# Optimization experiments

Hardware: AMD Instinct MI355X
Metric: run time of the kernel (lower is better)

## Reference

```python
import jax, jax.numpy as jnp
import numpy as np

KS, ST, PD = 4, 2, 1
AZI = 2.0 * np.pi / 1024.0
INC = 0.0073
C_IN, C_OUT = 64, 128


def _buffers():
    # torch: cos_azi[sh, sw] = cos(azi * (sw - ks//2)); cos_inc[sh, sw] = cos(inc * (sh - ks//2))
    d = np.arange(KS, dtype=np.float32) - KS // 2
    cos_azi = np.broadcast_to(np.cos(AZI * d)[None, :], (KS, KS))
    sin_azi = np.broadcast_to(np.sin(AZI * d)[None, :], (KS, KS))
    cos_inc = np.broadcast_to(np.cos(INC * d)[:, None], (KS, KS))
    sin_inc = np.broadcast_to(np.sin(INC * d)[:, None], (KS, KS))
    shp = (1, 1, 1, 1, KS, KS)
    return tuple(jnp.asarray(np.ascontiguousarray(b).reshape(shp), jnp.float32)
                 for b in (cos_azi, sin_azi, cos_inc, sin_inc))


def _pad(a, w_value):
    # pad width with constant, then height circularly (matches F.pad order in torch code)
    a = jnp.pad(a, ((0, 0), (0, 0), (0, 0), (PD, PD)), constant_values=w_value)
    return jnp.pad(a, ((0, 0), (0, 0), (PD, PD), (0, 0)), mode='wrap')


def _unfold(a):
    # torch a.unfold(3, ks, st).unfold(2, ks, st) -> [B,C,Ho,Wo,kw,kh]
    B, C, Hp, Wp = a.shape
    Ho = (Hp - KS) // ST + 1
    Wo = (Wp - KS) // ST + 1
    ih = (ST * jnp.arange(Ho))[:, None] + jnp.arange(KS)  # [Ho, ks]
    iw = (ST * jnp.arange(Wo))[:, None] + jnp.arange(KS)  # [Wo, ks]
    p = a[:, :, ih[:, None, :, None], iw[None, :, None, :]]  # [B,C,Ho,Wo,kh,kw]
    return jnp.transpose(p, (0, 1, 2, 3, 5, 4))               # [B,C,Ho,Wo,kw,kh]


def _forward(x, r, W1, b1, W2, b2, Wc, bc):
    cos_azi, sin_azi, cos_inc, sin_inc = _buffers()
    rp = _unfold(_pad(r, 100.0))                      # [B,1,Ho,Wo,kw,kh]
    r_center = rp[:, :, :, :, KS // 2, KS // 2]       # [B,1,Ho,Wo]
    pe0 = rp * cos_azi * cos_inc - r_center[..., None, None]
    pe1 = rp * cos_azi * sin_inc
    pe2 = rp * sin_azi
    pe = jnp.concatenate([pe0, pe1, pe2], axis=1)     # [B,3,Ho,Wo,kw,kh]
    pe = jnp.transpose(pe, (0, 2, 3, 4, 5, 1))        # [B,Ho,Wo,kw,kh,3]
    h = jax.nn.leaky_relu(pe @ W1 + b1, 0.2)          # [B,Ho,Wo,kw,kh,C]
    w = h @ W2 + b2                                   # [B,Ho,Wo,kw,kh,C]
    w = jnp.transpose(w, (0, 5, 1, 2, 3, 4))          # [B,C,Ho,Wo,kw,kh]
    xp = _unfold(_pad(x, 0.0)) * w                    # [B,C,Ho,Wo,kw,kh]
    B, C, Ho, Wo = xp.shape[:4]
    xp = jnp.transpose(xp, (0, 1, 4, 5, 2, 3)).reshape(B, C * KS * KS, Ho, Wo)
    out = jnp.einsum('bkhw,ok->bohw', xp, Wc) + bc[None, :, None, None]
    return out, r_center


def setup_inputs() -> dict:
    key = jax.random.key(0)
    ks = jax.random.split(key, 8)
    B, H, W = 4, 64, 1024
    x = jax.random.normal(ks[0], (B, C_IN, H, W), jnp.float32)
    r = jax.random.uniform(ks[1], (B, 1, H, W), jnp.float32) * 50.0  # metres
    W1 = jax.random.normal(ks[2], (3, C_IN), jnp.float32) * 0.3
    b1 = jax.random.normal(ks[3], (C_IN,), jnp.float32) * 0.02
    W2 = jax.random.normal(ks[4], (C_IN, C_IN), jnp.float32) * (1.0 / np.sqrt(C_IN))
    b2 = jax.random.normal(ks[5], (C_IN,), jnp.float32) * 0.02
    Wc = jax.random.normal(ks[6], (C_OUT, C_IN * KS * KS), jnp.float32) * (1.0 / np.sqrt(C_IN * KS * KS))
    bc = jax.random.normal(ks[7], (C_OUT,), jnp.float32) * 0.02
    return {'x': x, 'r': r, 'W1': W1, 'b1': b1, 'W2': W2, 'b2': b2, 'Wc': Wc, 'bc': bc}


def reference(x, r, W1, b1, W2, b2, Wc, bc):
    return _forward(x, r, W1, b1, W2, b2, Wc, bc)
```

## Files before the change

### kernel.cpp

```cpp
#include <hip/hip_runtime.h>
#include <hip/hip_bf16.h>

namespace {

constexpr int B_   = 4;
constexpr int CIN  = 64;
constexpr int COUT = 128;
constexpr int HIN  = 64,  WIN  = 1024;
constexpr int HOUT = 32,  WOUT = 512;
constexpr int TW   = 16;
constexpr int SP   = 1096;
constexpr int KTOT = CIN * 16;

typedef __bf16 bf16x8 __attribute__((ext_vector_type(8)));
typedef float  f32x4  __attribute__((ext_vector_type(4)));

__global__ void cvt_wts(const float* __restrict__ Wc, const float* __restrict__ W2,
                        __hip_bfloat16* __restrict__ wcb, __hip_bfloat16* __restrict__ w2t) {
    int i = blockIdx.x * 256 + threadIdx.x;
    if (i < COUT * KTOT) {
        int o = i >> 10, k = i & 1023, tap = k >> 6, c = k & 63;
        wcb[i] = __float2bfloat16(Wc[(size_t)o * KTOT + c * 16 + tap]);
    } else if (i < COUT * KTOT + CIN * CIN) {
        int m = i - COUT * KTOT;
        int c = m >> 6, c1 = m & 63;
        w2t[m] = __float2bfloat16(W2[c1 * CIN + c]);
    }
}

__global__ __launch_bounds__(256, 3)
void fused_ccconv(const float* __restrict__ x,  const float* __restrict__ r,
                  const float* __restrict__ W1, const float* __restrict__ b1,
                  const __hip_bfloat16* __restrict__ W2T, const float* __restrict__ b2,
                  const __hip_bfloat16* __restrict__ WcB, const float* __restrict__ bc,
                  float* __restrict__ out)
{
    __shared__ __hip_bfloat16 S[TW * SP];

    const int t   = threadIdx.x;
    const int bx  = blockIdx.x;
    const int wt  = bx & 31;
    const int ho  = (bx >> 5) & 31;
    const int b   = bx >> 10;
    const int wo0 = wt * TW;

    const float* rb = r + (size_t)b * HIN * WIN;

    if (t < TW) {
        const int wo = wo0 + t;
        out[(size_t)B_*COUT*HOUT*WOUT + ((size_t)b*HOUT + ho)*WOUT + wo] =
            rb[(2*ho + 1)*WIN + (2*wo + 1)];
    }

    const int ln   = t & 63;
    const int wv   = t >> 6;
    const int lm   = ln & 15;
    const int quad = ln >> 4;

    const float AZI = 0.006135923151542565f;
    const float INC = 0.0073f;

    {
        bf16x8 bfr[4][2];
        float  b2v[4];
        #pragma unroll
        for (int nt = 0; nt < 4; ++nt) {
            #pragma unroll
            for (int ks = 0; ks < 2; ++ks)
                bfr[nt][ks] = *reinterpret_cast<const bf16x8*>(
                    W2T + (nt*16 + lm)*CIN + ks*32 + quad*8);
            b2v[nt] = b2[nt*16 + lm];
        }

        const int i_ = lm >> 2, j_ = lm & 3;
        const float di = (float)(i_ - 2), dj = (float)(j_ - 2);
        const float cA = cosf(AZI * dj), sA = sinf(AZI * dj);
        const float cI = cosf(INC * di), sI = sinf(INC * di);
        const int hsrc = (2*ho + j_ + 63) & 63;

        #pragma unroll
        for (int mt = 0; mt < 4; ++mt) {
            const int p  = wv*4 + mt;
            const int wo = wo0 + p;
            const int wsrc = 2*wo + i_ - 1;
            const bool inb = (unsigned)wsrc < (unsigned)WIN;
            const float rpv = inb ? rb[hsrc*WIN + wsrc] : 100.0f;
            const float rc  = rb[(2*ho + 1)*WIN + (2*wo + 1)];
            const float pe0 = rpv * cA * cI - rc;
            const float pe1 = rpv * cA * sI;
            const float pe2 = rpv * sA;

            bf16x8 af0, af1;
            #pragma unroll
            for (int ks = 0; ks < 2; ++ks) {
                const int cb = ks*32 + quad*8;
                #pragma unroll
                for (int j = 0; j < 8; ++j) {
                    const int c1 = cb + j;
                    float hv = fmaf(pe0, W1[c1],
                               fmaf(pe1, W1[CIN + c1],
                               fmaf(pe2, W1[2*CIN + c1], b1[c1])));
                    hv = (hv >= 0.0f) ? hv : 0.2f * hv;
                    __hip_bfloat16 hb = __float2bfloat16(hv);
                    if (ks == 0) af0[j] = *reinterpret_cast<__bf16*>(&hb);
                    else         af1[j] = *reinterpret_cast<__bf16*>(&hb);
                }
            }

            #pragma unroll
            for (int nt = 0; nt < 4; ++nt) {
                f32x4 acc = {b2v[nt], b2v[nt], b2v[nt], b2v[nt]};
                acc = __builtin_amdgcn_mfma_f32_16x16x32_bf16(af0, bfr[nt][0], acc, 0, 0, 0);
                acc = __builtin_amdgcn_mfma_f32_16x16x32_bf16(af1, bfr[nt][1], acc, 0, 0, 0);
                #pragma unroll
                for (int q = 0; q < 4; ++q)
                    S[p*SP + (quad*4 + q)*68 + nt*16 + lm] = __float2bfloat16(acc[q]);
            }
        }
    }

    {
        const int p   = t >> 4;
        const int tap = t & 15;
        const int i_  = tap >> 2, j_ = tap & 3;
        const int hsrc = (2*ho + j_ + 63) & 63;
        const int wo   = wo0 + p;
        const int wsrc = 2*wo + i_ - 1;
        const bool inb = (unsigned)wsrc < (unsigned)WIN;

        uint2 wrow[16];
        const uint2* wp = reinterpret_cast<const uint2*>(S + p*SP + tap*68);
        #pragma unroll
        for (int u = 0; u < 16; ++u) wrow[u] = wp[u];

        const float* xb = x + (size_t)b*CIN*HIN*WIN + hsrc*WIN + wsrc;

        float xall[CIN];
        #pragma unroll
        for (int c = 0; c < CIN; ++c)
            xall[c] = inb ? xb[(size_t)c * HIN * WIN] : 0.0f;

        uint4* Ap = reinterpret_cast<uint4*>(S + p*SP + tap*64);
        #pragma unroll
        for (int g = 0; g < 8; ++g) {
            uint pk[4];
            #pragma unroll
            for (int pr = 0; pr < 4; ++pr) {
                const int c0 = g*8 + pr*2;
                const uint2 wv2 = wrow[c0 >> 2];
                const uint word = (c0 & 2) ? wv2.y : wv2.x;
                const float w0 = __uint_as_float(word << 16);
                const float w1 = __uint_as_float(word & 0xffff0000u);
                __hip_bfloat16 p0 = __float2bfloat16(w0 * xall[c0]);
                __hip_bfloat16 p1 = __float2bfloat16(w1 * xall[c0 + 1]);
                const uint lo = *reinterpret_cast<unsigned short*>(&p0);
                const uint hi = *reinterpret_cast<unsigned short*>(&p1);
                pk[pr] = lo | (hi << 16);
            }
            Ap[g] = make_uint4(pk[0], pk[1], pk[2], pk[3]);
        }
    }

    __syncthreads();

    {
        const int o0 = wv * 32;
        const __hip_bfloat16* wcP0 = WcB + ((size_t)(o0 + lm)) * KTOT + quad*8;
        const __hip_bfloat16* wcP1 = wcP0 + (size_t)16 * KTOT;
        const __hip_bfloat16* aP   = S + lm*SP + quad*8;

        f32x4 acc0 = {0.f,0.f,0.f,0.f};
        f32x4 acc1 = {0.f,0.f,0.f,0.f};

        #pragma unroll 4
        for (int ks = 0; ks < KTOT/32; ++ks) {
            const bf16x8 af = *reinterpret_cast<const bf16x8*>(aP   + ks*32);
            const bf16x8 w0 = *reinterpret_cast<const bf16x8*>(wcP0 + ks*32);
            const bf16x8 w1 = *reinterpret_cast<const bf16x8*>(wcP1 + ks*32);
            acc0 = __builtin_amdgcn_mfma_f32_16x16x32_bf16(w0, af, acc0, 0, 0, 0);
            acc1 = __builtin_amdgcn_mfma_f32_16x16x32_bf16(w1, af, acc1, 0, 0, 0);
        }

        #pragma unroll
        for (int q = 0; q < 4; ++q) {
            const int oa = o0 + quad*4 + q;
            const int ob = oa + 16;
            out[(((size_t)b*COUT + oa)*HOUT + ho)*WOUT + wo0 + lm] = acc0[q] + bc[oa];
            out[(((size_t)b*COUT + ob)*HOUT + ho)*WOUT + wo0 + lm] = acc1[q] + bc[ob];
        }
    }
}

}

extern "C" void kernel_launch(void* const* d_in, const int* in_sizes, int n_in,
                              void* d_out, int out_size, void* d_ws, size_t ws_size,
                              hipStream_t stream) {
    const float* x  = (const float*)d_in[0];
    const float* r  = (const float*)d_in[1];
    const float* W1 = (const float*)d_in[2];
    const float* b1 = (const float*)d_in[3];
    const float* W2 = (const float*)d_in[4];
    const float* b2 = (const float*)d_in[5];
    const float* Wc = (const float*)d_in[6];
    const float* bc = (const float*)d_in[7];
    float* out = (float*)d_out;

    __hip_bfloat16* wcb = (__hip_bfloat16*)d_ws;
    __hip_bfloat16* w2t = (__hip_bfloat16*)((char*)d_ws + 262144);

    const int ntot = COUT*KTOT + CIN*CIN;
    hipLaunchKernelGGL(cvt_wts, dim3((ntot + 255)/256), dim3(256), 0, stream,
                       Wc, W2, wcb, w2t);

    dim3 grid(B_ * HOUT * (WOUT / TW));
    dim3 block(256);
    hipLaunchKernelGGL(fused_ccconv, grid, block, 0, stream,
                       x, r, W1, b1, w2t, b2, wcb, bc, out);
}
```

Measured before the change: 289.2 us.

## Pre-transpose x to channel-last bf16 and swizzle shared-memory A tile

Adds a prep kernel that transposes x from NCHW fp32 into an NHWC bf16 workspace buffer, so the main kernel loads 64 channels per tap as eight contiguous 16-byte vectors instead of 64 strided scalar loads. It also XOR-swizzles the layout of the A tile in shared memory to cut bank conflicts in the MFMA loop, and raises the occupancy hint from 3 to 4 blocks. The cost is an extra full pass over x plus a bf16 round of x before the multiply. A fallback kernel handles the case where the workspace is too small.

```diff
diff --git a/kernel.cpp b/kernel.cpp
--- a/kernel.cpp
+++ b/kernel.cpp
@@ -28,12 +28,46 @@
     }
 }
 
-__global__ __launch_bounds__(256, 3)
-void fused_ccconv(const float* __restrict__ x,  const float* __restrict__ r,
-                  const float* __restrict__ W1, const float* __restrict__ b1,
-                  const __hip_bfloat16* __restrict__ W2T, const float* __restrict__ b2,
-                  const __hip_bfloat16* __restrict__ WcB, const float* __restrict__ bc,
-                  float* __restrict__ out)
+__global__ __launch_bounds__(256)
+void prep_xt(const float* __restrict__ x, __hip_bfloat16* __restrict__ xT) {
+    __shared__ float tile[CIN][65];
+    const int bx = blockIdx.x;
+    const int wt = bx & 15;
+    const int h  = (bx >> 4) & 63;
+    const int b  = bx >> 10;
+    const int w0 = wt * 64;
+    const int t  = threadIdx.x;
+
+    const int wl = t & 63;
+    const int c0 = (t >> 6) * 16;
+    #pragma unroll
+    for (int cc = 0; cc < 16; ++cc) {
+        const int c = c0 + cc;
+        tile[c][wl] = x[(((size_t)b*CIN + c)*HIN + h)*WIN + w0 + wl];
+    }
+    __syncthreads();
+
+    const int wl2 = t >> 2;
+    const int cq  = (t & 3) * 16;
+    __align__(16) unsigned short pack[16];
+    #pragma unroll
+    for (int cc = 0; cc < 16; ++cc) {
+        __hip_bfloat16 v = __float2bfloat16(tile[cq + cc][wl2]);
+        pack[cc] = *reinterpret_cast<unsigned short*>(&v);
+    }
+    uint4* dst = reinterpret_cast<uint4*>(
+        xT + ((size_t)(b*HIN + h)*WIN + w0 + wl2)*CIN + cq);
+    dst[0] = *reinterpret_cast<uint4*>(&pack[0]);
+    dst[1] = *reinterpret_cast<uint4*>(&pack[8]);
+}
+
+__global__ __launch_bounds__(256, 4)
+void fused_main(const float* __restrict__ r,
+                const float* __restrict__ W1, const float* __restrict__ b1,
+                const __hip_bfloat16* __restrict__ W2T, const float* __restrict__ b2,
+                const __hip_bfloat16* __restrict__ WcB, const float* __restrict__ bc,
+                const __hip_bfloat16* __restrict__ xT,
+                float* __restrict__ out)
 {
     __shared__ __hip_bfloat16 S[TW * SP];
 
@@ -128,36 +162,41 @@
         const int wsrc = 2*wo + i_ - 1;
         const bool inb = (unsigned)wsrc < (unsigned)WIN;
 
+        const __hip_bfloat16* xrow =
+            xT + ((size_t)(b*HIN + hsrc)*WIN + (inb ? wsrc : 0))*CIN;
+
+        uint4 xv[8];
+        #pragma unroll
+        for (int g = 0; g < 8; ++g)
+            xv[g] = inb ? reinterpret_cast<const uint4*>(xrow)[g]
+                        : make_uint4(0u,0u,0u,0u);
+
         uint2 wrow[16];
         const uint2* wp = reinterpret_cast<const uint2*>(S + p*SP + tap*68);
         #pragma unroll
         for (int u = 0; u < 16; ++u) wrow[u] = wp[u];
 
-        const float* xb = x + (size_t)b*CIN*HIN*WIN + hsrc*WIN + wsrc;
-
-        float xall[CIN];
-        #pragma unroll
-        for (int c = 0; c < CIN; ++c)
-            xall[c] = inb ? xb[(size_t)c * HIN * WIN] : 0.0f;
-
-        uint4* Ap = reinterpret_cast<uint4*>(S + p*SP + tap*64);
+        uint4* Ap = reinterpret_cast<uint4*>(S + (size_t)p*SP);
         #pragma unroll
         for (int g = 0; g < 8; ++g) {
             uint pk[4];
+            const unsigned short* xs = reinterpret_cast<const unsigned short*>(&xv[g]);
             #pragma unroll
             for (int pr = 0; pr < 4; ++pr) {
                 const int c0 = g*8 + pr*2;
                 const uint2 wv2 = wrow[c0 >> 2];
                 const uint word = (c0 & 2) ? wv2.y : wv2.x;
-                const float w0 = __uint_as_float(word << 16);
-                const float w1 = __uint_as_float(word & 0xffff0000u);
-                __hip_bfloat16 p0 = __float2bfloat16(w0 * xall[c0]);
-                __hip_bfloat16 p1 = __float2bfloat16(w1 * xall[c0 + 1]);
-                const uint lo = *reinterpret_cast<unsigned short*>(&p0);
-                const uint hi = *reinterpret_cast<unsigned short*>(&p1);
-                pk[pr] = lo | (hi << 16);
-            }
-            Ap[g] = make_uint4(pk[0], pk[1], pk[2], pk[3]);
+                const float w0f = __uint_as_float(word << 16);
+                const float w1f = __uint_as_float(word & 0xffff0000u);
+                const float x0f = __uint_as_float(((uint)xs[pr*2])   << 16);
+                const float x1f = __uint_as_float(((uint)xs[pr*2+1]) << 16);
+                __hip_bfloat16 p0 = __float2bfloat16(w0f * x0f);
+                __hip_bfloat16 p1 = __float2bfloat16(w1f * x1f);
+                pk[pr] = (uint)*reinterpret_cast<unsigned short*>(&p0)
+                       | ((uint)*reinterpret_cast<unsigned short*>(&p1) << 16);
+            }
+            const int pc = tap*8 + (g ^ (tap & 7));
+            Ap[pc] = make_uint4(pk[0], pk[1], pk[2], pk[3]);
         }
     }
 
@@ -167,14 +206,175 @@
         const int o0 = wv * 32;
         const __hip_bfloat16* wcP0 = WcB + ((size_t)(o0 + lm)) * KTOT + quad*8;
         const __hip_bfloat16* wcP1 = wcP0 + (size_t)16 * KTOT;
-        const __hip_bfloat16* aP   = S + lm*SP + quad*8;
+        const __hip_bfloat16* aBase = S + lm*SP;
 
         f32x4 acc0 = {0.f,0.f,0.f,0.f};
         f32x4 acc1 = {0.f,0.f,0.f,0.f};
 
         #pragma unroll 4
         for (int ks = 0; ks < KTOT/32; ++ks) {
-            const bf16x8 af = *reinterpret_cast<const bf16x8*>(aP   + ks*32);
+            const int s    = (ks >> 1) & 7;
+            const int phys = 8*(ks >> 1) + ((4*(ks & 1) + quad) ^ s);
+            const bf16x8 af = *reinterpret_cast<const bf16x8*>(aBase + phys*8);
+            const bf16x8 w0 = *reinterpret_cast<const bf16x8*>(wcP0 + ks*32);
+            const bf16x8 w1 = *reinterpret_cast<const bf16x8*>(wcP1 + ks*32);
+            acc0 = __builtin_amdgcn_mfma_f32_16x16x32_bf16(w0, af, acc0, 0, 0, 0);
+            acc1 = __builtin_amdgcn_mfma_f32_16x16x32_bf16(w1, af, acc1, 0, 0, 0);
+        }
+
+        #pragma unroll
+        for (int q = 0; q < 4; ++q) {
+            const int oa = o0 + quad*4 + q;
+            const int ob = oa + 16;
+            out[(((size_t)b*COUT + oa)*HOUT + ho)*WOUT + wo0 + lm] = acc0[q] + bc[oa];
+            out[(((size_t)b*COUT + ob)*HOUT + ho)*WOUT + wo0 + lm] = acc1[q] + bc[ob];
+        }
+    }
+}
+
+__global__ __launch_bounds__(256, 3)
+void fused_fb(const float* __restrict__ x,  const float* __restrict__ r,
+              const float* __restrict__ W1, const float* __restrict__ b1,
+              const __hip_bfloat16* __restrict__ W2T, const float* __restrict__ b2,
+              const __hip_bfloat16* __restrict__ WcB, const float* __restrict__ bc,
+              float* __restrict__ out)
+{
+    __shared__ __hip_bfloat16 S[TW * SP];
+
+    const int t   = threadIdx.x;
+    const int bx  = blockIdx.x;
+    const int wt  = bx & 31;
+    const int ho  = (bx >> 5) & 31;
+    const int b   = bx >> 10;
+    const int wo0 = wt * TW;
+
+    const float* rb = r + (size_t)b * HIN * WIN;
+
+    if (t < TW) {
+        const int wo = wo0 + t;
+        out[(size_t)B_*COUT*HOUT*WOUT + ((size_t)b*HOUT + ho)*WOUT + wo] =
+            rb[(2*ho + 1)*WIN + (2*wo + 1)];
+    }
+
+    const int ln   = t & 63;
+    const int wv   = t >> 6;
+    const int lm   = ln & 15;
+    const int quad = ln >> 4;
+
+    const float AZI = 0.006135923151542565f;
+    const float INC = 0.0073f;
+
+    {
+        bf16x8 bfr[4][2];
+        float  b2v[4];
+        #pragma unroll
+        for (int nt = 0; nt < 4; ++nt) {
+            #pragma unroll
+            for (int ks = 0; ks < 2; ++ks)
+                bfr[nt][ks] = *reinterpret_cast<const bf16x8*>(
+                    W2T + (nt*16 + lm)*CIN + ks*32 + quad*8);
+            b2v[nt] = b2[nt*16 + lm];
+        }
+        const int i_ = lm >> 2, j_ = lm & 3;
+        const float di = (float)(i_ - 2), dj = (float)(j_ - 2);
+        const float cA = cosf(AZI * dj), sA = sinf(AZI * dj);
+        const float cI = cosf(INC * di), sI = sinf(INC * di);
+        const int hsrc = (2*ho + j_ + 63) & 63;
+
+        #pragma unroll
+        for (int mt = 0; mt < 4; ++mt) {
+            const int p  = wv*4 + mt;
+            const int wo = wo0 + p;
+            const int wsrc = 2*wo + i_ - 1;
+            const bool inb = (unsigned)wsrc < (unsigned)WIN;
+            const float rpv = inb ? rb[hsrc*WIN + wsrc] : 100.0f;
+            const float rc  = rb[(2*ho + 1)*WIN + (2*wo + 1)];
+            const float pe0 = rpv * cA * cI - rc;
+            const float pe1 = rpv * cA * sI;
+            const float pe2 = rpv * sA;
+
+            bf16x8 af0, af1;
+            #pragma unroll
+            for (int ks = 0; ks < 2; ++ks) {
+                const int cb = ks*32 + quad*8;
+                #pragma unroll
+                for (int j = 0; j < 8; ++j) {
+                    const int c1 = cb + j;
+                    float hv = fmaf(pe0, W1[c1],
+                               fmaf(pe1, W1[CIN + c1],
+                               fmaf(pe2, W1[2*CIN + c1], b1[c1])));
+                    hv = (hv >= 0.0f) ? hv : 0.2f * hv;
+                    __hip_bfloat16 hb = __float2bfloat16(hv);
+                    if (ks == 0) af0[j] = *reinterpret_cast<__bf16*>(&hb);
+                    else         af1[j] = *reinterpret_cast<__bf16*>(&hb);
+                }
+            }
+            #pragma unroll
+            for (int nt = 0; nt < 4; ++nt) {
+                f32x4 acc = {b2v[nt], b2v[nt], b2v[nt], b2v[nt]};
+                acc = __builtin_amdgcn_mfma_f32_16x16x32_bf16(af0, bfr[nt][0], acc, 0, 0, 0);
+                acc = __builtin_amdgcn_mfma_f32_16x16x32_bf16(af1, bfr[nt][1], acc, 0, 0, 0);
+                #pragma unroll
+                for (int q = 0; q < 4; ++q)
+                    S[p*SP + (quad*4 + q)*68 + nt*16 + lm] = __float2bfloat16(acc[q]);
+            }
+        }
+    }
+
+    {
+        const int p   = t >> 4;
+        const int tap = t & 15;
+        const int i_  = tap >> 2, j_ = tap & 3;
+        const int hsrc = (2*ho + j_ + 63) & 63;
+        const int wo   = wo0 + p;
+        const int wsrc = 2*wo + i_ - 1;
+        const bool inb = (unsigned)wsrc < (unsigned)WIN;
+
+        uint2 wrow[16];
+        const uint2* wp = reinterpret_cast<const uint2*>(S + p*SP + tap*68);
+        #pragma unroll
+        for (int u = 0; u < 16; ++u) wrow[u] = wp[u];
+
+        const float* xb = x + (size_t)b*CIN*HIN*WIN + hsrc*WIN + wsrc;
+        uint4* Ap = reinterpret_cast<uint4*>(S + (size_t)p*SP);
+        #pragma unroll
+        for (int g = 0; g < 8; ++g) {
+            uint pk[4];
+            #pragma unroll
+            for (int pr = 0; pr < 4; ++pr) {
+                const int c0 = g*8 + pr*2;
+                const uint2 wv2 = wrow[c0 >> 2];
+                const uint word = (c0 & 2) ? wv2.y : wv2.x;
+                const float w0f = __uint_as_float(word << 16);
+                const float w1f = __uint_as_float(word & 0xffff0000u);
+                const float x0f = inb ? xb[(size_t)(c0    ) * HIN * WIN] : 0.0f;
+                const float x1f = inb ? xb[(size_t)(c0 + 1) * HIN * WIN] : 0.0f;
+                __hip_bfloat16 p0 = __float2bfloat16(w0f * x0f);
+                __hip_bfloat16 p1 = __float2bfloat16(w1f * x1f);
+                pk[pr] = (uint)*reinterpret_cast<unsigned short*>(&p0)
+                       | ((uint)*reinterpret_cast<unsigned short*>(&p1) << 16);
+            }
+            const int pc = tap*8 + (g ^ (tap & 7));
+            Ap[pc] = make_uint4(pk[0], pk[1], pk[2], pk[3]);
+        }
+    }
+
+    __syncthreads();
+
+    {
+        const int o0 = wv * 32;
+        const __hip_bfloat16* wcP0 = WcB + ((size_t)(o0 + lm)) * KTOT + quad*8;
+        const __hip_bfloat16* wcP1 = wcP0 + (size_t)16 * KTOT;
+        const __hip_bfloat16* aBase = S + lm*SP;
+
+        f32x4 acc0 = {0.f,0.f,0.f,0.f};
+        f32x4 acc1 = {0.f,0.f,0.f,0.f};
+
+        #pragma unroll 4
+        for (int ks = 0; ks < KTOT/32; ++ks) {
+            const int s    = (ks >> 1) & 7;
+            const int phys = 8*(ks >> 1) + ((4*(ks & 1) + quad) ^ s);
+            const bf16x8 af = *reinterpret_cast<const bf16x8*>(aBase + phys*8);
             const bf16x8 w0 = *reinterpret_cast<const bf16x8*>(wcP0 + ks*32);
             const bf16x8 w1 = *reinterpret_cast<const bf16x8*>(wcP1 + ks*32);
             acc0 = __builtin_amdgcn_mfma_f32_16x16x32_bf16(w0, af, acc0, 0, 0, 0);
@@ -208,6 +408,10 @@
 
     __hip_bfloat16* wcb = (__hip_bfloat16*)d_ws;
     __hip_bfloat16* w2t = (__hip_bfloat16*)((char*)d_ws + 262144);
+    __hip_bfloat16* xTp = (__hip_bfloat16*)((char*)d_ws + 524288);
+
+    const size_t XT_BYTES = (size_t)B_ * HIN * WIN * CIN * 2;
+    const bool use_xt = ws_size >= 524288 + XT_BYTES;
 
     const int ntot = COUT*KTOT + CIN*CIN;
     hipLaunchKernelGGL(cvt_wts, dim3((ntot + 255)/256), dim3(256), 0, stream,
@@ -215,6 +419,13 @@
 
     dim3 grid(B_ * HOUT * (WOUT / TW));
     dim3 block(256);
-    hipLaunchKernelGGL(fused_ccconv, grid, block, 0, stream,
-                       x, r, W1, b1, w2t, b2, wcb, bc, out);
-}
+
+    if (use_xt) {
+        hipLaunchKernelGGL(prep_xt, dim3(B_ * HIN * (WIN/64)), dim3(256), 0, stream, x, xTp);
+        hipLaunchKernelGGL(fused_main, grid, block, 0, stream,
+                           r, W1, b1, w2t, b2, wcb, bc, xTp, out);
+    } else {
+        hipLaunchKernelGGL(fused_fb, grid, block, 0, stream,
+                           x, r, W1, b1, w2t, b2, wcb, bc, out);
+    }
+}
```

Result: slower. 300.2 us (+3.8%).
